# Kernel optimization log

Hardware: AMD Instinct MI355X
Metric: run time of the kernel (lower is better)

## Reference

```python
import jax, jax.numpy as jnp
import numpy as np

NEG = -9e15   # mask value used by reference pyGAT implementation
ALPHA = 0.2   # LeakyReLU negative slope
B, N, F_IN, H, F_HID = 131072, 8, 30, 3, 8


def setup_inputs() -> dict:
    key = jax.random.key(0)
    ks = jax.random.split(key, 14)
    x = jax.random.normal(ks[0], (B, N, F_IN), jnp.float32)
    adj = (jax.random.uniform(ks[1], (B, N, N)) > 0.5).astype(jnp.float32)
    adj = jnp.maximum(adj, jnp.eye(N, dtype=jnp.float32))  # self loops

    def init(k, shp, fan):
        return jax.random.normal(k, shp, jnp.float32) * np.float32(1.0 / np.sqrt(fan))

    return {
        "x": x,
        "adj": adj,
        "W_heads": init(ks[2], (H, F_IN, F_HID), F_IN),       # per-head W
        "a_heads": init(ks[3], (H, 2 * F_HID), 2 * F_HID),    # per-head attention vec
        "W_out": init(ks[4], (H * F_HID, 1), H * F_HID),      # out_att W (nclass=1)
        "a_out": init(ks[5], (2,), 2),                          # out_att attention vec
        "mu_W": init(ks[6], (8, 8), 8), "mu_b": jnp.zeros((8,), jnp.float32),
        "sg_W": init(ks[7], (8, 8), 8), "sg_b": jnp.zeros((8,), jnp.float32),
        "v_W": init(ks[8], (1, 8), 8), "v_b": jnp.zeros((1,), jnp.float32),
    }


def _gat(x, adj, W_heads, a_heads, W_out, a_out):
    # --- multi-head layer (concat=True) ---
    Wh = jnp.einsum('bnf,hfo->bhno', x, W_heads)            # [B,H,N,F_HID]
    a1, a2 = a_heads[:, :F_HID], a_heads[:, F_HID:]
    f1 = jnp.einsum('bhno,ho->bhn', Wh, a1)
    f2 = jnp.einsum('bhno,ho->bhn', Wh, a2)
    e = jax.nn.leaky_relu(f1[:, :, :, None] + f2[:, :, None, :], ALPHA)  # [B,H,N,N]
    e = jnp.where(adj[:, None, :, :] > 0, e, NEG)
    att = jax.nn.softmax(e, axis=-1)
    h = jax.nn.elu(jnp.einsum('bhnm,bhmo->bhno', att, Wh))  # [B,H,N,F_HID]
    h = h.transpose(0, 2, 1, 3).reshape(x.shape[0], N, H * F_HID)  # concat heads

    # --- output attention layer (concat=False, nclass=1) ---
    Wh2 = h @ W_out                                          # [B,N,1]
    g1 = Wh2[..., 0] * a_out[0]
    g2 = Wh2[..., 0] * a_out[1]
    e2 = jax.nn.leaky_relu(g1[:, :, None] + g2[:, None, :], ALPHA)  # [B,N,N]
    e2 = jnp.where(adj > 0, e2, NEG)
    att2 = jax.nn.softmax(e2, axis=-1)
    out = jnp.einsum('bnm,bmo->bno', att2, Wh2)              # [B,N,1]
    return jax.nn.elu(out)[..., 0]                            # squeeze(-1) -> [B,8]


def reference(x, adj, W_heads, a_heads, W_out, a_out,
              mu_W, mu_b, sg_W, sg_b, v_W, v_b):
    g = _gat(x, adj, W_heads, a_heads, W_out, a_out)          # [B,8]
    mu = jax.nn.sigmoid(g @ mu_W.T + mu_b)                    # [B,8]
    sigma = jax.nn.softplus(g @ sg_W.T + sg_b) + 0.001        # [B,8]
    value = g @ v_W.T + v_b                                   # [B,1]
    return (mu, sigma, value)
```

## Files before the change

### kernel.cpp

```cpp
#include <hip/hip_runtime.h>
#include <math.h>

#define TPB 128

constexpr int Bn    = 131072;
constexpr float LOG2E = 1.4426950408889634f;

typedef float v2f __attribute__((ext_vector_type(2)));

__global__ __launch_bounds__(TPB)
void gat_ppo_kernel(const float* __restrict__ xg,
                    const float* __restrict__ adjg,
                    const float* __restrict__ Wg,
                    const float* __restrict__ ahg,
                    const float* __restrict__ wog,
                    const float* __restrict__ aog,
                    const float* __restrict__ muWg,
                    const float* __restrict__ mubg,
                    const float* __restrict__ sgWg,
                    const float* __restrict__ sgbg,
                    const float* __restrict__ vWg,
                    const float* __restrict__ vbg,
                    float* __restrict__ outg)
{
    __shared__ float4 tile[2 * 200];

    const int lb = threadIdx.x;
    const int w  = lb >> 6;
    const int g  = (lb & 63) >> 3;
    const int n  = lb & 7;
    const size_t t = (size_t)blockIdx.x * TPB + lb;

    float4* wt4 = tile + w * 200;

    unsigned amask;
    {
        const float4* a4 = (const float4*)(adjg) + t * 2;
        float4 a0 = a4[0], a1 = a4[1];
        amask =  (unsigned)(a0.x > 0.0f)
              | ((unsigned)(a0.y > 0.0f) << 1)
              | ((unsigned)(a0.z > 0.0f) << 2)
              | ((unsigned)(a0.w > 0.0f) << 3)
              | ((unsigned)(a1.x > 0.0f) << 4)
              | ((unsigned)(a1.y > 0.0f) << 5)
              | ((unsigned)(a1.z > 0.0f) << 6)
              | ((unsigned)(a1.w > 0.0f) << 7);
    }

    float x[30];
    {
        const float2* xr = (const float2*)(xg + t * 30);
        #pragma unroll
        for (int k = 0; k < 15; ++k) {
            float2 v = xr[k];
            x[2 * k] = v.x; x[2 * k + 1] = v.y;
        }
    }

    const v2f* Wp = (const v2f*)Wg;
    float wh2 = 0.0f;

    #pragma unroll
    for (int h = 0; h < 3; ++h) {
        v2f acc[4];
        #pragma unroll
        for (int o2 = 0; o2 < 4; ++o2) acc[o2] = (v2f){0.0f, 0.0f};
        #pragma unroll
        for (int f = 0; f < 30; ++f) {
            v2f xf = (v2f){x[f], x[f]};
            #pragma unroll
            for (int o2 = 0; o2 < 4; ++o2)
                acc[o2] = __builtin_elementwise_fma(xf, Wp[h * 120 + f * 4 + o2], acc[o2]);
        }

        float s1 = 0.0f, s2 = 0.0f;
        #pragma unroll
        for (int o2 = 0; o2 < 4; ++o2) {
            s1 = fmaf(acc[o2].x, ahg[h * 16 + 2 * o2],     s1);
            s1 = fmaf(acc[o2].y, ahg[h * 16 + 2 * o2 + 1], s1);
            s2 = fmaf(acc[o2].x, ahg[h * 16 + 8 + 2 * o2],     s2);
            s2 = fmaf(acc[o2].y, ahg[h * 16 + 8 + 2 * o2 + 1], s2);
        }
        float f1h = s1 * LOG2E;
        float f2h = s2 * LOG2E;

        wt4[g * 25 + n * 3]     = (float4){acc[0].x, acc[0].y, acc[1].x, acc[1].y};
        wt4[g * 25 + n * 3 + 1] = (float4){acc[2].x, acc[2].y, acc[3].x, acc[3].y};

        float p[8];
        float s = 0.0f;
        #pragma unroll
        for (int m = 0; m < 8; ++m) {
            float ev = f1h + __shfl(f2h, m, 8);
            ev = fmaxf(ev, 0.2f * ev);
            float pe = ((amask >> m) & 1u) ? __builtin_amdgcn_exp2f(ev) : 0.0f;
            p[m] = pe; s += pe;
        }

        v2f hacc[4];
        #pragma unroll
        for (int o2 = 0; o2 < 4; ++o2) hacc[o2] = (v2f){0.0f, 0.0f};
        #pragma unroll
        for (int m = 0; m < 8; ++m) {
            float4 lo = wt4[g * 25 + m * 3];
            float4 hi = wt4[g * 25 + m * 3 + 1];
            v2f av = (v2f){p[m], p[m]};
            hacc[0] = __builtin_elementwise_fma(av, (v2f){lo.x, lo.y}, hacc[0]);
            hacc[1] = __builtin_elementwise_fma(av, (v2f){lo.z, lo.w}, hacc[1]);
            hacc[2] = __builtin_elementwise_fma(av, (v2f){hi.x, hi.y}, hacc[2]);
            hacc[3] = __builtin_elementwise_fma(av, (v2f){hi.z, hi.w}, hacc[3]);
        }
        float rs = 1.0f / s;
        #pragma unroll
        for (int o2 = 0; o2 < 4; ++o2) {
            #pragma unroll
            for (int j = 0; j < 2; ++j) {
                float hv = hacc[o2][j] * rs;
                hv = (hv > 0.0f) ? hv : (__expf(hv) - 1.0f);
                wh2 = fmaf(hv, wog[h * 8 + 2 * o2 + j], wh2);
            }
        }
    }

    const float a0c = aog[0] * LOG2E, a1c = aog[1] * LOG2E;
    float wh2a[8];
    #pragma unroll
    for (int m = 0; m < 8; ++m) wh2a[m] = __shfl(wh2, m, 8);

    float g1 = a0c * wh2;
    float s2s = 0.0f;
    float og = 0.0f;
    #pragma unroll
    for (int m = 0; m < 8; ++m) {
        float ev = fmaf(a1c, wh2a[m], g1);
        ev = fmaxf(ev, 0.2f * ev);
        float pe = ((amask >> m) & 1u) ? __builtin_amdgcn_exp2f(ev) : 0.0f;
        s2s += pe;
        og = fmaf(pe, wh2a[m], og);
    }
    og /= s2s;
    float g2v = (og > 0.0f) ? og : (__expf(og) - 1.0f);

    v2f gp[4];
    #pragma unroll
    for (int m = 0; m < 4; ++m)
        gp[m] = (v2f){__shfl(g2v, 2 * m, 8), __shfl(g2v, 2 * m + 1, 8)};

    const v2f* muWp = (const v2f*)muWg;
    const v2f* sgWp = (const v2f*)sgWg;
    const v2f* vWp  = (const v2f*)vWg;
    v2f ma = (v2f){0.0f, 0.0f}, sa = (v2f){0.0f, 0.0f}, va = (v2f){0.0f, 0.0f};
    #pragma unroll
    for (int k = 0; k < 4; ++k) {
        ma = __builtin_elementwise_fma(gp[k], muWp[n * 4 + k], ma);
        sa = __builtin_elementwise_fma(gp[k], sgWp[n * 4 + k], sa);
        va = __builtin_elementwise_fma(gp[k], vWp[k],          va);
    }
    float mu = ma.x + ma.y + mubg[n];
    float sg = sa.x + sa.y + sgbg[n];
    float vv = va.x + va.y + vbg[0];

    mu = 1.0f / (1.0f + __expf(-mu));
    sg = fmaxf(sg, 0.0f) + log1pf(__expf(-fabsf(sg))) + 0.001f;

    outg[t]          = mu;
    outg[Bn * 8 + t] = sg;
    if (n == 0) outg[Bn * 16 + (t >> 3)] = vv;
}

extern "C" void kernel_launch(void* const* d_in, const int* in_sizes, int n_in,
                              void* d_out, int out_size, void* d_ws, size_t ws_size,
                              hipStream_t stream) {
    const float* xg   = (const float*)d_in[0];
    const float* adjg = (const float*)d_in[1];
    const float* Wg   = (const float*)d_in[2];
    const float* ahg  = (const float*)d_in[3];
    const float* wog  = (const float*)d_in[4];
    const float* aog  = (const float*)d_in[5];
    const float* muW  = (const float*)d_in[6];
    const float* mub  = (const float*)d_in[7];
    const float* sgW  = (const float*)d_in[8];
    const float* sgb  = (const float*)d_in[9];
    const float* vW   = (const float*)d_in[10];
    const float* vb   = (const float*)d_in[11];
    float* outg = (float*)d_out;

    dim3 grid(Bn * 8 / TPB);
    gat_ppo_kernel<<<grid, TPB, 0, stream>>>(xg, adjg, Wg, ahg, wog, aog,
                                             muW, mub, sgW, sgb, vW, vb, outg);
}
```

Baseline: 49.99 us.

## Use persistent grid-stride blocks with software prefetch of next x/adj

Replaces the one-thread-per-node grid (8192 blocks of 128 threads) with 1024 blocks of 256 threads. Each block loops over 4 chunks and loads the next chunk's x row and adjacency row into registers while it computes the current one. The goal is to hide global load latency and cut block launch overhead. The price is higher register pressure (30 extra floats plus 8 adj values per thread), which may lower occupancy or cause spills.

New measurement: 88.19 us. +76.4%, slower.

```diff
diff --git a/kernel.cpp b/kernel.cpp
--- a/kernel.cpp
+++ b/kernel.cpp
@@ -1,7 +1,9 @@
 #include <hip/hip_runtime.h>
 #include <math.h>
 
-#define TPB 128
+#define TPB  256
+#define NBLK 1024
+#define NIT  4
 
 constexpr int Bn    = 131072;
 constexpr float LOG2E = 1.4426950408889634f;
@@ -23,31 +25,20 @@
                     const float* __restrict__ vbg,
                     float* __restrict__ outg)
 {
-    __shared__ float4 tile[2 * 200];
+    __shared__ float4 tile[4 * 200];
 
     const int lb = threadIdx.x;
     const int w  = lb >> 6;
     const int g  = (lb & 63) >> 3;
     const int n  = lb & 7;
-    const size_t t = (size_t)blockIdx.x * TPB + lb;
 
     float4* wt4 = tile + w * 200;
-
-    unsigned amask;
-    {
-        const float4* a4 = (const float4*)(adjg) + t * 2;
-        float4 a0 = a4[0], a1 = a4[1];
-        amask =  (unsigned)(a0.x > 0.0f)
-              | ((unsigned)(a0.y > 0.0f) << 1)
-              | ((unsigned)(a0.z > 0.0f) << 2)
-              | ((unsigned)(a0.w > 0.0f) << 3)
-              | ((unsigned)(a1.x > 0.0f) << 4)
-              | ((unsigned)(a1.y > 0.0f) << 5)
-              | ((unsigned)(a1.z > 0.0f) << 6)
-              | ((unsigned)(a1.w > 0.0f) << 7);
-    }
+    const v2f* Wp = (const v2f*)Wg;
+
+    size_t t = (size_t)blockIdx.x * TPB + lb;
 
     float x[30];
+    float4 a0, a1;
     {
         const float2* xr = (const float2*)(xg + t * 30);
         #pragma unroll
@@ -55,117 +46,150 @@
             float2 v = xr[k];
             x[2 * k] = v.x; x[2 * k + 1] = v.y;
         }
+        const float4* a4 = (const float4*)(adjg) + t * 2;
+        a0 = a4[0]; a1 = a4[1];
     }
 
-    const v2f* Wp = (const v2f*)Wg;
-    float wh2 = 0.0f;
-
-    #pragma unroll
-    for (int h = 0; h < 3; ++h) {
-        v2f acc[4];
-        #pragma unroll
-        for (int o2 = 0; o2 < 4; ++o2) acc[o2] = (v2f){0.0f, 0.0f};
-        #pragma unroll
-        for (int f = 0; f < 30; ++f) {
-            v2f xf = (v2f){x[f], x[f]};
-            #pragma unroll
-            for (int o2 = 0; o2 < 4; ++o2)
-                acc[o2] = __builtin_elementwise_fma(xf, Wp[h * 120 + f * 4 + o2], acc[o2]);
-        }
-
-        float s1 = 0.0f, s2 = 0.0f;
-        #pragma unroll
-        for (int o2 = 0; o2 < 4; ++o2) {
-            s1 = fmaf(acc[o2].x, ahg[h * 16 + 2 * o2],     s1);
-            s1 = fmaf(acc[o2].y, ahg[h * 16 + 2 * o2 + 1], s1);
-            s2 = fmaf(acc[o2].x, ahg[h * 16 + 8 + 2 * o2],     s2);
-            s2 = fmaf(acc[o2].y, ahg[h * 16 + 8 + 2 * o2 + 1], s2);
-        }
-        float f1h = s1 * LOG2E;
-        float f2h = s2 * LOG2E;
-
-        wt4[g * 25 + n * 3]     = (float4){acc[0].x, acc[0].y, acc[1].x, acc[1].y};
-        wt4[g * 25 + n * 3 + 1] = (float4){acc[2].x, acc[2].y, acc[3].x, acc[3].y};
-
-        float p[8];
-        float s = 0.0f;
+    #pragma unroll 1
+    for (int it = 0; it < NIT; ++it) {
+        const size_t tn = t + (size_t)NBLK * TPB;
+        float xn[30];
+        float4 b0, b1;
+        if (it + 1 < NIT) {
+            const float2* xr = (const float2*)(xg + tn * 30);
+            #pragma unroll
+            for (int k = 0; k < 15; ++k) {
+                float2 v = xr[k];
+                xn[2 * k] = v.x; xn[2 * k + 1] = v.y;
+            }
+            const float4* a4 = (const float4*)(adjg) + tn * 2;
+            b0 = a4[0]; b1 = a4[1];
+        }
+
+        const unsigned amask =
+              (unsigned)(a0.x > 0.0f)
+            | ((unsigned)(a0.y > 0.0f) << 1)
+            | ((unsigned)(a0.z > 0.0f) << 2)
+            | ((unsigned)(a0.w > 0.0f) << 3)
+            | ((unsigned)(a1.x > 0.0f) << 4)
+            | ((unsigned)(a1.y > 0.0f) << 5)
+            | ((unsigned)(a1.z > 0.0f) << 6)
+            | ((unsigned)(a1.w > 0.0f) << 7);
+
+        float wh2 = 0.0f;
+        #pragma unroll
+        for (int h = 0; h < 3; ++h) {
+            v2f acc[4];
+            #pragma unroll
+            for (int o2 = 0; o2 < 4; ++o2) acc[o2] = (v2f){0.0f, 0.0f};
+            #pragma unroll
+            for (int f = 0; f < 30; ++f) {
+                v2f xf = (v2f){x[f], x[f]};
+                #pragma unroll
+                for (int o2 = 0; o2 < 4; ++o2)
+                    acc[o2] = __builtin_elementwise_fma(xf, Wp[h * 120 + f * 4 + o2], acc[o2]);
+            }
+
+            float s1 = 0.0f, s2 = 0.0f;
+            #pragma unroll
+            for (int o2 = 0; o2 < 4; ++o2) {
+                s1 = fmaf(acc[o2].x, ahg[h * 16 + 2 * o2],     s1);
+                s1 = fmaf(acc[o2].y, ahg[h * 16 + 2 * o2 + 1], s1);
+                s2 = fmaf(acc[o2].x, ahg[h * 16 + 8 + 2 * o2],     s2);
+                s2 = fmaf(acc[o2].y, ahg[h * 16 + 8 + 2 * o2 + 1], s2);
+            }
+            float f1h = s1 * LOG2E;
+            float f2h = s2 * LOG2E;
+
+            wt4[g * 25 + n * 3]     = (float4){acc[0].x, acc[0].y, acc[1].x, acc[1].y};
+            wt4[g * 25 + n * 3 + 1] = (float4){acc[2].x, acc[2].y, acc[3].x, acc[3].y};
+
+            float p[8];
+            float s = 0.0f;
+            #pragma unroll
+            for (int m = 0; m < 8; ++m) {
+                float ev = f1h + __shfl(f2h, m, 8);
+                ev = fmaxf(ev, 0.2f * ev);
+                float pe = ((amask >> m) & 1u) ? __builtin_amdgcn_exp2f(ev) : 0.0f;
+                p[m] = pe; s += pe;
+            }
+
+            v2f hacc[4];
+            #pragma unroll
+            for (int o2 = 0; o2 < 4; ++o2) hacc[o2] = (v2f){0.0f, 0.0f};
+            #pragma unroll
+            for (int m = 0; m < 8; ++m) {
+                float4 lo = wt4[g * 25 + m * 3];
+                float4 hi = wt4[g * 25 + m * 3 + 1];
+                v2f av = (v2f){p[m], p[m]};
+                hacc[0] = __builtin_elementwise_fma(av, (v2f){lo.x, lo.y}, hacc[0]);
+                hacc[1] = __builtin_elementwise_fma(av, (v2f){lo.z, lo.w}, hacc[1]);
+                hacc[2] = __builtin_elementwise_fma(av, (v2f){hi.x, hi.y}, hacc[2]);
+                hacc[3] = __builtin_elementwise_fma(av, (v2f){hi.z, hi.w}, hacc[3]);
+            }
+            float rs = 1.0f / s;
+            #pragma unroll
+            for (int o2 = 0; o2 < 4; ++o2) {
+                #pragma unroll
+                for (int j = 0; j < 2; ++j) {
+                    float hv = hacc[o2][j] * rs;
+                    hv = (hv > 0.0f) ? hv : (__expf(hv) - 1.0f);
+                    wh2 = fmaf(hv, wog[h * 8 + 2 * o2 + j], wh2);
+                }
+            }
+        }
+
+        const float a0c = aog[0] * LOG2E, a1c = aog[1] * LOG2E;
+        float wh2a[8];
+        #pragma unroll
+        for (int m = 0; m < 8; ++m) wh2a[m] = __shfl(wh2, m, 8);
+
+        float g1 = a0c * wh2;
+        float s2s = 0.0f, og = 0.0f;
         #pragma unroll
         for (int m = 0; m < 8; ++m) {
-            float ev = f1h + __shfl(f2h, m, 8);
+            float ev = fmaf(a1c, wh2a[m], g1);
             ev = fmaxf(ev, 0.2f * ev);
             float pe = ((amask >> m) & 1u) ? __builtin_amdgcn_exp2f(ev) : 0.0f;
-            p[m] = pe; s += pe;
-        }
-
-        v2f hacc[4];
-        #pragma unroll
-        for (int o2 = 0; o2 < 4; ++o2) hacc[o2] = (v2f){0.0f, 0.0f};
-        #pragma unroll
-        for (int m = 0; m < 8; ++m) {
-            float4 lo = wt4[g * 25 + m * 3];
-            float4 hi = wt4[g * 25 + m * 3 + 1];
-            v2f av = (v2f){p[m], p[m]};
-            hacc[0] = __builtin_elementwise_fma(av, (v2f){lo.x, lo.y}, hacc[0]);
-            hacc[1] = __builtin_elementwise_fma(av, (v2f){lo.z, lo.w}, hacc[1]);
-            hacc[2] = __builtin_elementwise_fma(av, (v2f){hi.x, hi.y}, hacc[2]);
-            hacc[3] = __builtin_elementwise_fma(av, (v2f){hi.z, hi.w}, hacc[3]);
-        }
-        float rs = 1.0f / s;
-        #pragma unroll
-        for (int o2 = 0; o2 < 4; ++o2) {
-            #pragma unroll
-            for (int j = 0; j < 2; ++j) {
-                float hv = hacc[o2][j] * rs;
-                hv = (hv > 0.0f) ? hv : (__expf(hv) - 1.0f);
-                wh2 = fmaf(hv, wog[h * 8 + 2 * o2 + j], wh2);
-            }
+            s2s += pe;
+            og = fmaf(pe, wh2a[m], og);
+        }
+        og /= s2s;
+        float g2v = (og > 0.0f) ? og : (__expf(og) - 1.0f);
+
+        v2f gp[4];
+        #pragma unroll
+        for (int m = 0; m < 4; ++m)
+            gp[m] = (v2f){__shfl(g2v, 2 * m, 8), __shfl(g2v, 2 * m + 1, 8)};
+
+        const v2f* muWp = (const v2f*)muWg;
+        const v2f* sgWp = (const v2f*)sgWg;
+        const v2f* vWp  = (const v2f*)vWg;
+        v2f ma = (v2f){0.0f, 0.0f}, sa = (v2f){0.0f, 0.0f}, va = (v2f){0.0f, 0.0f};
+        #pragma unroll
+        for (int k = 0; k < 4; ++k) {
+            ma = __builtin_elementwise_fma(gp[k], muWp[n * 4 + k], ma);
+            sa = __builtin_elementwise_fma(gp[k], sgWp[n * 4 + k], sa);
+            va = __builtin_elementwise_fma(gp[k], vWp[k],          va);
+        }
+        float mu = ma.x + ma.y + mubg[n];
+        float sg = sa.x + sa.y + sgbg[n];
+        float vv = va.x + va.y + vbg[0];
+
+        mu = 1.0f / (1.0f + __expf(-mu));
+        sg = fmaxf(sg, 0.0f) + log1pf(__expf(-fabsf(sg))) + 0.001f;
+
+        outg[t]          = mu;
+        outg[Bn * 8 + t] = sg;
+        if (n == 0) outg[Bn * 16 + (t >> 3)] = vv;
+
+        if (it + 1 < NIT) {
+            #pragma unroll
+            for (int k = 0; k < 30; ++k) x[k] = xn[k];
+            a0 = b0; a1 = b1;
+            t = tn;
         }
     }
-
-    const float a0c = aog[0] * LOG2E, a1c = aog[1] * LOG2E;
-    float wh2a[8];
-    #pragma unroll
-    for (int m = 0; m < 8; ++m) wh2a[m] = __shfl(wh2, m, 8);
-
-    float g1 = a0c * wh2;
-    float s2s = 0.0f;
-    float og = 0.0f;
-    #pragma unroll
-    for (int m = 0; m < 8; ++m) {
-        float ev = fmaf(a1c, wh2a[m], g1);
-        ev = fmaxf(ev, 0.2f * ev);
-        float pe = ((amask >> m) & 1u) ? __builtin_amdgcn_exp2f(ev) : 0.0f;
-        s2s += pe;
-        og = fmaf(pe, wh2a[m], og);
-    }
-    og /= s2s;
-    float g2v = (og > 0.0f) ? og : (__expf(og) - 1.0f);
-
-    v2f gp[4];
-    #pragma unroll
-    for (int m = 0; m < 4; ++m)
-        gp[m] = (v2f){__shfl(g2v, 2 * m, 8), __shfl(g2v, 2 * m + 1, 8)};
-
-    const v2f* muWp = (const v2f*)muWg;
-    const v2f* sgWp = (const v2f*)sgWg;
-    const v2f* vWp  = (const v2f*)vWg;
-    v2f ma = (v2f){0.0f, 0.0f}, sa = (v2f){0.0f, 0.0f}, va = (v2f){0.0f, 0.0f};
-    #pragma unroll
-    for (int k = 0; k < 4; ++k) {
-        ma = __builtin_elementwise_fma(gp[k], muWp[n * 4 + k], ma);
-        sa = __builtin_elementwise_fma(gp[k], sgWp[n * 4 + k], sa);
-        va = __builtin_elementwise_fma(gp[k], vWp[k],          va);
-    }
-    float mu = ma.x + ma.y + mubg[n];
-    float sg = sa.x + sa.y + sgbg[n];
-    float vv = va.x + va.y + vbg[0];
-
-    mu = 1.0f / (1.0f + __expf(-mu));
-    sg = fmaxf(sg, 0.0f) + log1pf(__expf(-fabsf(sg))) + 0.001f;
-
-    outg[t]          = mu;
-    outg[Bn * 8 + t] = sg;
-    if (n == 0) outg[Bn * 16 + (t >> 3)] = vv;
 }
 
 extern "C" void kernel_launch(void* const* d_in, const int* in_sizes, int n_in,
@@ -185,7 +209,7 @@
     const float* vb   = (const float*)d_in[11];
     float* outg = (float*)d_out;
 
-    dim3 grid(Bn * 8 / TPB);
+    dim3 grid(NBLK);
     gat_ppo_kernel<<<grid, TPB, 0, stream>>>(xg, adjg, Wg, ahg, wog, aog,
                                              muW, mub, sgW, sgb, vW, vb, outg);
 }
```
